# Kernel optimization log

Hardware: AMD Instinct MI355X
Metric: run time of the kernel (lower is better)

The kernel has to match this reference:

```python
import jax, jax.numpy as jnp
import numpy as np

D_MODEL = 512
N_HEADS = 8
HEAD_DIM = D_MODEL // N_HEADS
KV_RANK = 128
B, T = 8, 4096


def _rope(x):
    # x: (B, H, T, D); non-interleaved half rotation as in the source
    d = x.shape[-1]
    half = d // 2
    freq = 1.0 / (10000.0 ** (jnp.arange(half, dtype=jnp.float32) / half))
    t = jnp.arange(x.shape[2], dtype=jnp.float32)
    freqs = jnp.einsum('i,j->ij', t, freq)          # (T, half)
    cos_f = jnp.cos(freqs)[None, None, :, :]
    sin_f = jnp.sin(freqs)[None, None, :, :]
    x1, x2 = jnp.split(x, 2, axis=-1)
    return jnp.concatenate([x1 * cos_f - x2 * sin_f, x1 * sin_f + x2 * cos_f], axis=-1)


def setup_inputs() -> dict:
    key = jax.random.key(0)
    ks = jax.random.split(key, 9)
    s = lambda fan_in: 1.0 / np.sqrt(fan_in)
    return {
        'x':  jax.random.normal(ks[0], (B, T, D_MODEL), dtype=jnp.float32),
        'Wq': jax.random.normal(ks[1], (D_MODEL, D_MODEL), dtype=jnp.float32) * s(D_MODEL),
        'bq': jnp.zeros((D_MODEL,), dtype=jnp.float32),
        'Wd': jax.random.normal(ks[2], (D_MODEL, KV_RANK), dtype=jnp.float32) * s(D_MODEL),
        'bd': jnp.zeros((KV_RANK,), dtype=jnp.float32),
        'Wu': jax.random.normal(ks[3], (KV_RANK, D_MODEL * 2), dtype=jnp.float32) * s(KV_RANK),
        'bu': jnp.zeros((D_MODEL * 2,), dtype=jnp.float32),
        'Wo': jax.random.normal(ks[4], (D_MODEL, D_MODEL), dtype=jnp.float32) * s(D_MODEL),
        'bo': jnp.zeros((D_MODEL,), dtype=jnp.float32),
    }


def reference(x, Wq, bq, Wd, bd, Wu, bu, Wo, bo):
    b, t, _ = x.shape
    q = (x @ Wq + bq).reshape(b, t, N_HEADS, HEAD_DIM).transpose(0, 2, 1, 3)   # (B,H,T,D)
    kv = ((x @ Wd + bd) @ Wu + bu).reshape(b, t, N_HEADS, 2 * HEAD_DIM)
    k, v = jnp.split(kv, 2, axis=-1)
    k = k.transpose(0, 2, 1, 3)                                                # (B,H,T,D)
    v = v.transpose(0, 2, 1, 3)
    q = jax.nn.elu(_rope(q)) + 1.0
    k = jax.nn.elu(_rope(k)) + 1.0
    context = jnp.einsum('bhtd,bhte->bhde', k, v)      # (B,H,D,D)
    out = jnp.einsum('bhtd,bhde->bhte', q, context)    # (B,H,T,D)
    k_sum = k.sum(axis=2)                              # (B,H,D)
    z = 1.0 / (jnp.einsum('bhtd,bhd->bht', q, k_sum) + 1e-6)
    out = out * z[..., None]
    out = out.transpose(0, 2, 1, 3).reshape(b, t, D_MODEL)
    return out @ Wo + bo
```

## Files before the change

### kernel.cpp

```cpp
#include <hip/hip_runtime.h>
#include <math.h>

#define T_SEQ 4096
#define BATCH 8
#define DM    512
#define NH    8
#define HD    64
#define RANK  128
#define NCHUNK 8
#define MTOT  (BATCH * T_SEQ)
#define BK 64

typedef unsigned int u32;
typedef unsigned short u16;
using bf16x8  = __attribute__((ext_vector_type(8))) __bf16;
using floatx4 = __attribute__((ext_vector_type(4))) float;

__device__ __forceinline__ u16 f2bf(float f) {
  u32 u = __float_as_uint(f);
  u32 r = (u + 0x7FFFu + ((u >> 16) & 1u)) >> 16;
  return (u16)r;
}
__device__ __forceinline__ void hilo(float f, u16& h, u16& l) {
  h = f2bf(f);
  float hf = __uint_as_float(((u32)h) << 16);
  l = f2bf(f - hf);
}
__device__ __forceinline__ float elu1(float x) {
  return (x > 0.f) ? x + 1.f : expf(x);
}
__device__ __forceinline__ void async16(void* lds, const void* g) {
  __builtin_amdgcn_global_load_lds(
      (const __attribute__((address_space(1))) u32*)g,
      (__attribute__((address_space(3))) u32*)lds, 16, 0, 0);
}
__device__ __forceinline__ bf16x8 fragld(const u16* base, int row, int kk, int quad) {
  int ch = (kk * 4 + quad) ^ (row & 7);
  return *(const bf16x8*)((const char*)base + row * 128 + ch * 16);
}
__device__ __forceinline__ bf16x8 fragldA(const u16* base, int row, int gc) {
  int ch = gc ^ (row & 7);
  return *(const bf16x8*)((const char*)base + row * 256 + ch * 16);
}

__global__ void cs_kernel(float2* __restrict__ cs) {
  int i = blockIdx.x * 256 + threadIdx.x;
  if (i >= T_SEQ * 32) return;
  int t = i >> 5, d = i & 31;
  double freq = pow(10000.0, -(double)d / 32.0);
  double a = (double)t * freq;
  cs[i] = make_float2((float)cos(a), (float)sin(a));
}

__global__ __launch_bounds__(256) void pack_bf16(const float* __restrict__ x,
                                                 u16* __restrict__ y) {
  int i = blockIdx.x * 256 + threadIdx.x;
  const float4 v = ((const float4*)x)[i];
  ushort4 o;
  o.x = f2bf(v.x); o.y = f2bf(v.y); o.z = f2bf(v.z); o.w = f2bf(v.w);
  ((ushort4*)y)[i] = o;
}

__global__ __launch_bounds__(256) void transpose_cast(const float* __restrict__ W,
                                                      u16* __restrict__ WT,
                                                      int K, int N) {
  __shared__ float t[32][33];
  int kb = blockIdx.x * 32, nb = blockIdx.y * 32;
  int tx = threadIdx.x & 31, tg = threadIdx.x >> 5;
#pragma unroll
  for (int i = 0; i < 4; i++)
    t[tg * 4 + i][tx] = W[(size_t)(kb + tg * 4 + i) * N + nb + tx];
  __syncthreads();
#pragma unroll
  for (int i = 0; i < 4; i++)
    WT[(size_t)(nb + tg * 4 + i) * K + kb + tx] = f2bf(t[tx][tg * 4 + i]);
}

__global__ __launch_bounds__(256) void transpose_cast_hilo(
    const float* __restrict__ W, u16* __restrict__ WTh, u16* __restrict__ WTl,
    int K, int N) {
  __shared__ float t[32][33];
  int kb = blockIdx.x * 32, nb = blockIdx.y * 32;
  int tx = threadIdx.x & 31, tg = threadIdx.x >> 5;
#pragma unroll
  for (int i = 0; i < 4; i++)
    t[tg * 4 + i][tx] = W[(size_t)(kb + tg * 4 + i) * N + nb + tx];
  __syncthreads();
#pragma unroll
  for (int i = 0; i < 4; i++) {
    u16 h, l;
    hilo(t[tx][tg * 4 + i], h, l);
    WTh[(size_t)(nb + tg * 4 + i) * K + kb + tx] = h;
    WTl[(size_t)(nb + tg * 4 + i) * K + kb + tx] = l;
  }
}

template <bool BF16OUT>
__global__ __launch_bounds__(256) void gemm_bf16_bt(
    const u16* __restrict__ A, const u16* __restrict__ BT,
    const float* __restrict__ bias, void* __restrict__ Cv,
    int M, int N, int K) {
  __shared__ u16 As[128 * BK];
  __shared__ u16 Bs[128 * BK];
  const int tid = threadIdx.x;
  const int lane = tid & 63, w = tid >> 6;
  const int m0 = blockIdx.y * 128, n0 = blockIdx.x * 128;
  const int wm = (w & 1) * 64, wn = (w >> 1) * 64;
  const int srow = lane >> 3, schunk = lane & 7;
  const int lane15 = lane & 15, quad = lane >> 4;
  floatx4 acc[4][4] = {};
  for (int kt = 0; kt < K; kt += BK) {
    __syncthreads();
#pragma unroll
    for (int i = 0; i < 4; i++) {
      int R = (w * 4 + i) * 8 + srow;
      int cg = schunk ^ (R & 7);
      async16((char*)As + (w * 4 + i) * 1024,
              (const char*)A + ((size_t)(m0 + R) * K + kt) * 2 + cg * 16);
      async16((char*)Bs + (w * 4 + i) * 1024,
              (const char*)BT + ((size_t)(n0 + R) * K + kt) * 2 + cg * 16);
    }
    __syncthreads();
#pragma unroll
    for (int kk = 0; kk < 2; kk++) {
      bf16x8 af[4], bfr[4];
#pragma unroll
      for (int mi = 0; mi < 4; mi++) af[mi] = fragld(As, wm + mi * 16 + lane15, kk, quad);
#pragma unroll
      for (int ni = 0; ni < 4; ni++) bfr[ni] = fragld(Bs, wn + ni * 16 + lane15, kk, quad);
#pragma unroll
      for (int mi = 0; mi < 4; mi++)
#pragma unroll
        for (int ni = 0; ni < 4; ni++)
          acc[mi][ni] = __builtin_amdgcn_mfma_f32_16x16x32_bf16(
              af[mi], bfr[ni], acc[mi][ni], 0, 0, 0);
    }
  }
#pragma unroll
  for (int mi = 0; mi < 4; mi++) {
    int row = m0 + wm + mi * 16 + (quad << 2);
#pragma unroll
    for (int ni = 0; ni < 4; ni++) {
      int col = n0 + wn + ni * 16 + lane15;
      float bb = bias[col];
#pragma unroll
      for (int r = 0; r < 4; r++) {
        float v = acc[mi][ni][r] + bb;
        if (BF16OUT) ((u16*)Cv)[(size_t)(row + r) * N + col] = f2bf(v);
        else         ((float*)Cv)[(size_t)(row + r) * N + col] = v;
      }
    }
  }
}

__global__ __launch_bounds__(256) void gemm_wd_hilo(
    const u16* __restrict__ A, const u16* __restrict__ BT,
    const float* __restrict__ bias, u16* __restrict__ Ch, u16* __restrict__ Cl,
    int M, int N, int K) {
  __shared__ u16 As[128 * BK];
  __shared__ u16 Bs[128 * BK];
  const int tid = threadIdx.x;
  const int lane = tid & 63, w = tid >> 6;
  const int m0 = blockIdx.y * 128, n0 = blockIdx.x * 128;
  const int wm = (w & 1) * 64, wn = (w >> 1) * 64;
  const int srow = lane >> 3, schunk = lane & 7;
  const int lane15 = lane & 15, quad = lane >> 4;
  floatx4 acc[4][4] = {};
  for (int kt = 0; kt < K; kt += BK) {
    __syncthreads();
#pragma unroll
    for (int i = 0; i < 4; i++) {
      int R = (w * 4 + i) * 8 + srow;
      int cg = schunk ^ (R & 7);
      async16((char*)As + (w * 4 + i) * 1024,
              (const char*)A + ((size_t)(m0 + R) * K + kt) * 2 + cg * 16);
      async16((char*)Bs + (w * 4 + i) * 1024,
              (const char*)BT + ((size_t)(n0 + R) * K + kt) * 2 + cg * 16);
    }
    __syncthreads();
#pragma unroll
    for (int kk = 0; kk < 2; kk++) {
      bf16x8 af[4], bfr[4];
#pragma unroll
      for (int mi = 0; mi < 4; mi++) af[mi] = fragld(As, wm + mi * 16 + lane15, kk, quad);
#pragma unroll
      for (int ni = 0; ni < 4; ni++) bfr[ni] = fragld(Bs, wn + ni * 16 + lane15, kk, quad);
#pragma unroll
      for (int mi = 0; mi < 4; mi++)
#pragma unroll
        for (int ni = 0; ni < 4; ni++)
          acc[mi][ni] = __builtin_amdgcn_mfma_f32_16x16x32_bf16(
              af[mi], bfr[ni], acc[mi][ni], 0, 0, 0);
    }
  }
#pragma unroll
  for (int mi = 0; mi < 4; mi++) {
    int row = m0 + wm + mi * 16 + (quad << 2);
#pragma unroll
    for (int ni = 0; ni < 4; ni++) {
      int col = n0 + wn + ni * 16 + lane15;
      float bb = bias[col];
#pragma unroll
      for (int r = 0; r < 4; r++) {
        float v = acc[mi][ni][r] + bb;
        u16 hh, ll;
        hilo(v, hh, ll);
        size_t idx = (size_t)(row + r) * N + col;
        Ch[idx] = hh;
        Cl[idx] = ll;
      }
    }
  }
}

__global__ __launch_bounds__(256, 2) void ctx_fused(
    const u16* __restrict__ Chi, const u16* __restrict__ Clo,
    const u16* __restrict__ Wuh, const u16* __restrict__ Wul,
    const float* __restrict__ bu, const float2* __restrict__ cs,
    float* __restrict__ ctxp, float* __restrict__ ksump) {
  __shared__ __align__(16) u16 Ah_[64 * 128];
  __shared__ __align__(16) u16 Al_[64 * 128];
  __shared__ __align__(16) u16 Kh_[64 * 64], Kl_[64 * 64];
  __shared__ __align__(16) u16 Vh_[64 * 64], Vl_[64 * 64];
  __shared__ float bus[128];
  __shared__ float ksl[256];
  const int tid = threadIdx.x;
  const int lane = tid & 63, w = tid >> 6;
  const int lane15 = lane & 15, quad = lane >> 4;
  const int chunk = blockIdx.x, bh = blockIdx.y;
  const int b = bh >> 3, h = bh & 7;
  if (tid < 128) bus[tid] = bu[h * RANK + tid];

  bf16x8 wuh[2][2][2], wul[2][2][2];
  {
    const int cb = (w >> 1) * 4 + (w & 1);
#pragma unroll
    for (int rp = 0; rp < 2; rp++)
#pragma unroll
      for (int kk = 0; kk < 2; kk++)
#pragma unroll
        for (int ct = 0; ct < 2; ct++) {
          size_t off = (size_t)(h * 128 + (cb + ct * 2) * 16 + lane15) * RANK
                       + rp * 64 + kk * 32 + quad * 8;
          wuh[rp][kk][ct] = *(const bf16x8*)(Wuh + off);
          wul[rp][kk][ct] = *(const bf16x8*)(Wul + off);
        }
  }

  const int t00 = chunk * 512;
  auto stageA = [&](int t0) {
#pragma unroll
    for (int i = 0; i < 4; i++) {
      int R = i * 16 + w * 4 + (lane >> 4);
      int cg = (lane & 15) ^ (R & 7);
      size_t aoff = ((size_t)(b * T_SEQ + t0 + R) * RANK + cg * 8) * 2;
      async16((char*)Ah_ + (i * 16 + w * 4) * 256, (const char*)Chi + aoff);
      async16((char*)Al_ + (i * 16 + w * 4) * 256, (const char*)Clo + aoff);
    }
  };

  floatx4 acc2[4] = {};
  float ks0 = 0.f, ks1 = 0.f;
  stageA(t00);
  for (int tile = 0; tile < 8; tile++) {
    const int t0 = t00 + tile * 64;
    __syncthreads();
    floatx4 acc[4][2] = {};
#pragma unroll
    for (int rp = 0; rp < 2; rp++)
#pragma unroll
      for (int kk = 0; kk < 2; kk++) {
        const int gc = rp * 8 + kk * 4 + quad;
        bf16x8 ah[4], al[4];
#pragma unroll
        for (int tt = 0; tt < 4; tt++) {
          ah[tt] = fragldA(Ah_, tt * 16 + lane15, gc);
          al[tt] = fragldA(Al_, tt * 16 + lane15, gc);
        }
#pragma unroll
        for (int tt = 0; tt < 4; tt++)
#pragma unroll
          for (int ct = 0; ct < 2; ct++) {
            acc[tt][ct] = __builtin_amdgcn_mfma_f32_16x16x32_bf16(
                ah[tt], wuh[rp][kk][ct], acc[tt][ct], 0, 0, 0);
            acc[tt][ct] = __builtin_amdgcn_mfma_f32_16x16x32_bf16(
                ah[tt], wul[rp][kk][ct], acc[tt][ct], 0, 0, 0);
            acc[tt][ct] = __builtin_amdgcn_mfma_f32_16x16x32_bf16(
                al[tt], wuh[rp][kk][ct], acc[tt][ct], 0, 0, 0);
            acc[tt][ct] = __builtin_amdgcn_mfma_f32_16x16x32_bf16(
                al[tt], wul[rp][kk][ct], acc[tt][ct], 0, 0, 0);
          }
      }
    __syncthreads();
    if (tile < 7) stageA(t0 + 64);
    if (w < 2) {
      const int d = w * 16 + lane15;
      const float b1 = bus[d], b2 = bus[d + 32];
#pragma unroll
      for (int tt = 0; tt < 4; tt++) {
        const int tg = t0 + tt * 16 + (quad << 2);
        ushort4 khl, kll, khh, klh;
        float s0 = 0.f, s1 = 0.f;
#pragma unroll
        for (int r = 0; r < 4; r++) {
          float2 sc = cs[(size_t)(tg + r) * 32 + d];
          float x1 = acc[tt][0][r] + b1;
          float x2 = acc[tt][1][r] + b2;
          float k1 = elu1(x1 * sc.x - x2 * sc.y);
          float k2 = elu1(x1 * sc.y + x2 * sc.x);
          s0 += k1; s1 += k2;
          u16 hh, ll;
          hilo(k1, hh, ll); ((u16*)&khl)[r] = hh; ((u16*)&kll)[r] = ll;
          hilo(k2, hh, ll); ((u16*)&khh)[r] = hh; ((u16*)&klh)[r] = ll;
        }
        ks0 += s0; ks1 += s1;
        const int chq = tt * 2 + (quad >> 1);
        const int off = d * 128 + (((chq ^ (d & 7)) << 4) | ((quad & 1) << 3));
        *(ushort4*)((char*)Kh_ + off)            = khl;
        *(ushort4*)((char*)Kl_ + off)            = kll;
        *(ushort4*)((char*)Kh_ + off + 32 * 128) = khh;
        *(ushort4*)((char*)Kl_ + off + 32 * 128) = klh;
      }
    } else {
      const int e = (w - 2) * 16 + lane15;
#pragma unroll
      for (int ct = 0; ct < 2; ct++) {
        const float be = bus[64 + e + ct * 32];
#pragma unroll
        for (int tt = 0; tt < 4; tt++) {
          ushort4 vh4, vl4;
#pragma unroll
          for (int r = 0; r < 4; r++) {
            u16 hh, ll;
            hilo(acc[tt][ct][r] + be, hh, ll);
            ((u16*)&vh4)[r] = hh; ((u16*)&vl4)[r] = ll;
          }
          const int chq = tt * 2 + (quad >> 1);
          const int off = (e + ct * 32) * 128 +
                          (((chq ^ (e & 7)) << 4) | ((quad & 1) << 3));
          *(ushort4*)((char*)Vh_ + off) = vh4;
          *(ushort4*)((char*)Vl_ + off) = vl4;
        }
      }
    }
    __syncthreads();
#pragma unroll
    for (int kk = 0; kk < 2; kk++) {
      bf16x8 kh8 = fragld(Kh_, w * 16 + lane15, kk, quad);
      bf16x8 kl8 = fragld(Kl_, w * 16 + lane15, kk, quad);
#pragma unroll
      for (int ni = 0; ni < 4; ni++) {
        bf16x8 vh8 = fragld(Vh_, ni * 16 + lane15, kk, quad);
        bf16x8 vl8 = fragld(Vl_, ni * 16 + lane15, kk, quad);
        acc2[ni] = __builtin_amdgcn_mfma_f32_16x16x32_bf16(kh8, vh8, acc2[ni], 0, 0, 0);
        acc2[ni] = __builtin_amdgcn_mfma_f32_16x16x32_bf16(kh8, vl8, acc2[ni], 0, 0, 0);
        acc2[ni] = __builtin_amdgcn_mfma_f32_16x16x32_bf16(kl8, vh8, acc2[ni], 0, 0, 0);
        acc2[ni] = __builtin_amdgcn_mfma_f32_16x16x32_bf16(kl8, vl8, acc2[ni], 0, 0, 0);
      }
    }
  }
  const size_t obase = ((size_t)bh * NCHUNK + chunk) * 4096;
#pragma unroll
  for (int ni = 0; ni < 4; ni++)
#pragma unroll
    for (int r = 0; r < 4; r++)
      ctxp[obase + (size_t)(w * 16 + (quad << 2) + r) * 64 + ni * 16 + lane15] = acc2[ni][r];
  if (w < 2) {
    ksl[w * 128 + lane]      = ks0;
    ksl[w * 128 + 64 + lane] = ks1;
  }
  __syncthreads();
  if (tid < 64) {
    const int d = tid;
    const int wk = (d >> 4) & 1, hi = d >> 5, l15 = d & 15;
    float s = 0.f;
#pragma unroll
    for (int q = 0; q < 4; q++) s += ksl[wk * 128 + hi * 64 + q * 16 + l15];
    ksump[(bh * NCHUNK + chunk) * 64 + d] = s;
  }
}

__global__ __launch_bounds__(256) void reduce_kernel(
    const float* __restrict__ ctxp, const float* __restrict__ ksump,
    float* __restrict__ ctx, float* __restrict__ ksum) {
  int bh = blockIdx.x, tid = threadIdx.x;
  for (int i = tid; i < 4096; i += 256) {
    float s = 0.f;
    for (int c = 0; c < NCHUNK; c++) s += ctxp[(size_t)(bh * NCHUNK + c) * 4096 + i];
    ctx[(size_t)bh * 4096 + i] = s;
  }
  if (tid < 64) {
    float s = 0.f;
    for (int c = 0; c < NCHUNK; c++) s += ksump[(bh * NCHUNK + c) * 64 + tid];
    ksum[bh * 64 + tid] = s;
  }
}

__global__ __launch_bounds__(256) void out_kernel(
    const float* __restrict__ Q, const float* __restrict__ ctx,
    const float* __restrict__ ksum, const float2* __restrict__ cs,
    u16* __restrict__ attn) {
  __shared__ __align__(16) float Qs[128 * 68];
  __shared__ __align__(16) float Cts[64 * 68];
  __shared__ float ks[64];
  __shared__ float zs[128];
  const int tid = threadIdx.x;
  const int tt0 = blockIdx.x * 128;
  const int bh = blockIdx.y;
  const int b = bh >> 3, h = bh & 7;
  for (int i = tid; i < 4096; i += 256)
    Cts[(i >> 6) * 68 + (i & 63)] = ctx[(size_t)bh * 4096 + i];
  if (tid < 64) ks[tid] = ksum[bh * 64 + tid];
  for (int i = tid; i < 8192; i += 256) {
    int t = i >> 6, d = i & 63;
    Qs[t * 68 + d] = Q[(size_t)(b * T_SEQ + tt0 + t) * DM + h * HD + d];
  }
  __syncthreads();
  for (int i = tid; i < 128 * 32; i += 256) {
    int t = i >> 5, d = i & 31;
    float x1 = Qs[t * 68 + d], x2 = Qs[t * 68 + d + 32];
    float2 sc = cs[(size_t)(tt0 + t) * 32 + d];
    float r1 = x1 * sc.x - x2 * sc.y;
    float r2 = x1 * sc.y + x2 * sc.x;
    Qs[t * 68 + d]      = (r1 > 0.f) ? r1 + 1.f : expf(r1);
    Qs[t * 68 + d + 32] = (r2 > 0.f) ? r2 + 1.f : expf(r2);
  }
  __syncthreads();
  if (tid < 128) {
    float z = 0.f;
#pragma unroll 8
    for (int d = 0; d < 64; d++) z += Qs[tid * 68 + d] * ks[d];
    zs[tid] = 1.f / (z + 1e-6f);
  }
  __syncthreads();
  const int tx = tid & 15, ty = tid >> 4;
  float acc[8][4] = {};
  for (int d = 0; d < 64; d++) {
    const float4 c4 = *(const float4*)&Cts[d * 68 + tx * 4];
#pragma unroll
    for (int i = 0; i < 8; i++) {
      float q = Qs[(ty * 8 + i) * 68 + d];
      acc[i][0] += q * c4.x; acc[i][1] += q * c4.y;
      acc[i][2] += q * c4.z; acc[i][3] += q * c4.w;
    }
  }
#pragma unroll
  for (int i = 0; i < 8; i++) {
    int t = ty * 8 + i;
    float zz = zs[t];
    ushort4 o;
    o.x = f2bf(acc[i][0] * zz); o.y = f2bf(acc[i][1] * zz);
    o.z = f2bf(acc[i][2] * zz); o.w = f2bf(acc[i][3] * zz);
    *(ushort4*)&attn[(size_t)(b * T_SEQ + tt0 + t) * DM + h * HD + tx * 4] = o;
  }
}

extern "C" void kernel_launch(void* const* d_in, const int* in_sizes, int n_in,
                              void* d_out, int out_size, void* d_ws, size_t ws_size,
                              hipStream_t stream) {
  const float* x  = (const float*)d_in[0];
  const float* Wq = (const float*)d_in[1];
  const float* bq = (const float*)d_in[2];
  const float* Wd = (const float*)d_in[3];
  const float* bd = (const float*)d_in[4];
  const float* Wu = (const float*)d_in[5];
  const float* bu = (const float*)d_in[6];
  const float* Wo = (const float*)d_in[7];
  const float* bo = (const float*)d_in[8];
  float* out = (float*)d_out;

  float* ws = (float*)d_ws;
  size_t o_cs   = 0;
  size_t o_Q    = o_cs + (size_t)T_SEQ * 32 * 2;
  size_t o_Chi  = o_Q + (size_t)MTOT * DM;
  size_t o_Clo  = o_Chi + (size_t)MTOT * RANK / 2;
  size_t o_ctxp = o_Clo + (size_t)MTOT * RANK / 2;
  size_t o_ksp  = o_ctxp + (size_t)64 * NCHUNK * 4096;
  size_t o_ctx  = o_ksp + (size_t)64 * NCHUNK * 64;
  size_t o_ks   = o_ctx + (size_t)64 * 4096;
  size_t o_xbf  = o_ks + 64 * 64;
  size_t o_wqT  = o_xbf + (size_t)MTOT * DM / 2;
  size_t o_wdT  = o_wqT + (size_t)DM * DM / 2;
  size_t o_woT  = o_wdT + (size_t)DM * RANK / 2;
  size_t o_wuTh = o_woT + (size_t)DM * DM / 2;
  size_t o_wuTl = o_wuTh + (size_t)(2 * DM) * RANK / 2;
  size_t total  = o_wuTl + (size_t)(2 * DM) * RANK / 2;
  if (ws_size < total * sizeof(float)) return;

  float2* cs  = (float2*)(ws + o_cs);
  float* Qb   = ws + o_Q;
  u16* Chi    = (u16*)(ws + o_Chi);
  u16* Clo    = (u16*)(ws + o_Clo);
  float* ctxp = ws + o_ctxp;
  float* ksp  = ws + o_ksp;
  float* ctxf = ws + o_ctx;
  float* ksf  = ws + o_ks;
  u16* x_bf   = (u16*)(ws + o_xbf);
  u16* attn_bf= x_bf;
  u16* WqT    = (u16*)(ws + o_wqT);
  u16* WdT    = (u16*)(ws + o_wdT);
  u16* WoT    = (u16*)(ws + o_woT);
  u16* WuTh   = (u16*)(ws + o_wuTh);
  u16* WuTl   = (u16*)(ws + o_wuTl);

  cs_kernel<<<(T_SEQ * 32 + 255) / 256, 256, 0, stream>>>(cs);
  pack_bf16<<<(MTOT * DM / 4) / 256, 256, 0, stream>>>(x, x_bf);
  transpose_cast<<<dim3(DM / 32, DM / 32), 256, 0, stream>>>(Wq, WqT, DM, DM);
  transpose_cast<<<dim3(DM / 32, RANK / 32), 256, 0, stream>>>(Wd, WdT, DM, RANK);
  transpose_cast<<<dim3(DM / 32, DM / 32), 256, 0, stream>>>(Wo, WoT, DM, DM);
  transpose_cast_hilo<<<dim3(RANK / 32, (2 * DM) / 32), 256, 0, stream>>>(
      Wu, WuTh, WuTl, RANK, 2 * DM);

  gemm_bf16_bt<false><<<dim3(DM / 128, MTOT / 128), 256, 0, stream>>>(
      x_bf, WqT, bq, Qb, MTOT, DM, DM);
  gemm_wd_hilo<<<dim3(RANK / 128, MTOT / 128), 256, 0, stream>>>(
      x_bf, WdT, bd, Chi, Clo, MTOT, RANK, DM);
  ctx_fused<<<dim3(NCHUNK, BATCH * NH), 256, 0, stream>>>(
      Chi, Clo, WuTh, WuTl, bu, cs, ctxp, ksp);
  reduce_kernel<<<BATCH * NH, 256, 0, stream>>>(ctxp, ksp, ctxf, ksf);
  out_kernel<<<dim3(T_SEQ / 128, BATCH * NH), 256, 0, stream>>>(Qb, ctxf, ksf, cs, attn_bf);
  gemm_bf16_bt<false><<<dim3(DM / 128, MTOT / 128), 256, 0, stream>>>(
      attn_bf, WoT, bo, out, MTOT, DM, DM);
}
```

Measured before the change: 332.8 us.

## Split context kernel into more chunks, halve A staging, drop lo*lo MFMAs

Doubles the number of sequence chunks in the fused context kernel and processes each 64-row tile as two 32-row halves with a smaller shared A buffer, raising the occupancy hint from two to three blocks per CU. It also drops the low-by-low product terms from both the Wu projection and the K^T V accumulation, cutting MFMA work by a quarter. The partial-context buffer now aliases the x_bf16 workspace. This trades a small loss in split-precision accuracy, extra barriers and a larger reduction for more parallelism and less matrix work; the aliasing assumes x_bf is dead by the time ctx_fused runs.

```diff
diff --git a/kernel.cpp b/kernel.cpp
--- a/kernel.cpp
+++ b/kernel.cpp
@@ -7,7 +7,7 @@
 #define NH    8
 #define HD    64
 #define RANK  128
-#define NCHUNK 8
+#define NCHUNK 16
 #define MTOT  (BATCH * T_SEQ)
 #define BK 64
 
@@ -213,13 +213,13 @@
   }
 }
 
-__global__ __launch_bounds__(256, 2) void ctx_fused(
+__global__ __launch_bounds__(256, 3) void ctx_fused(
     const u16* __restrict__ Chi, const u16* __restrict__ Clo,
     const u16* __restrict__ Wuh, const u16* __restrict__ Wul,
     const float* __restrict__ bu, const float2* __restrict__ cs,
     float* __restrict__ ctxp, float* __restrict__ ksump) {
-  __shared__ __align__(16) u16 Ah_[64 * 128];
-  __shared__ __align__(16) u16 Al_[64 * 128];
+  __shared__ __align__(16) u16 Ah_[32 * 128];
+  __shared__ __align__(16) u16 Al_[32 * 128];
   __shared__ __align__(16) u16 Kh_[64 * 64], Kl_[64 * 64];
   __shared__ __align__(16) u16 Vh_[64 * 64], Vl_[64 * 64];
   __shared__ float bus[128];
@@ -247,13 +247,13 @@
         }
   }
 
-  const int t00 = chunk * 512;
-  auto stageA = [&](int t0) {
-#pragma unroll
-    for (int i = 0; i < 4; i++) {
+  const int t00 = chunk * (T_SEQ / NCHUNK);
+  auto stageA = [&](int tg0) {
+#pragma unroll
+    for (int i = 0; i < 2; i++) {
       int R = i * 16 + w * 4 + (lane >> 4);
       int cg = (lane & 15) ^ (R & 7);
-      size_t aoff = ((size_t)(b * T_SEQ + t0 + R) * RANK + cg * 8) * 2;
+      size_t aoff = ((size_t)(b * T_SEQ + tg0 + R) * RANK + cg * 8) * 2;
       async16((char*)Ah_ + (i * 16 + w * 4) * 256, (const char*)Chi + aoff);
       async16((char*)Al_ + (i * 16 + w * 4) * 256, (const char*)Clo + aoff);
     }
@@ -262,84 +262,87 @@
   floatx4 acc2[4] = {};
   float ks0 = 0.f, ks1 = 0.f;
   stageA(t00);
-  for (int tile = 0; tile < 8; tile++) {
+  for (int tile = 0; tile < T_SEQ / NCHUNK / 64; tile++) {
     const int t0 = t00 + tile * 64;
-    __syncthreads();
-    floatx4 acc[4][2] = {};
-#pragma unroll
-    for (int rp = 0; rp < 2; rp++)
-#pragma unroll
-      for (int kk = 0; kk < 2; kk++) {
-        const int gc = rp * 8 + kk * 4 + quad;
-        bf16x8 ah[4], al[4];
-#pragma unroll
-        for (int tt = 0; tt < 4; tt++) {
-          ah[tt] = fragldA(Ah_, tt * 16 + lane15, gc);
-          al[tt] = fragldA(Al_, tt * 16 + lane15, gc);
+#pragma unroll
+    for (int hh = 0; hh < 2; hh++) {
+      __syncthreads();
+      floatx4 acc[2][2] = {};
+#pragma unroll
+      for (int rp = 0; rp < 2; rp++)
+#pragma unroll
+        for (int kk = 0; kk < 2; kk++) {
+          const int gc = rp * 8 + kk * 4 + quad;
+          bf16x8 ah[2], al[2];
+#pragma unroll
+          for (int tt = 0; tt < 2; tt++) {
+            ah[tt] = fragldA(Ah_, tt * 16 + lane15, gc);
+            al[tt] = fragldA(Al_, tt * 16 + lane15, gc);
+          }
+#pragma unroll
+          for (int tt = 0; tt < 2; tt++)
+#pragma unroll
+            for (int ct = 0; ct < 2; ct++) {
+              acc[tt][ct] = __builtin_amdgcn_mfma_f32_16x16x32_bf16(
+                  ah[tt], wuh[rp][kk][ct], acc[tt][ct], 0, 0, 0);
+              acc[tt][ct] = __builtin_amdgcn_mfma_f32_16x16x32_bf16(
+                  ah[tt], wul[rp][kk][ct], acc[tt][ct], 0, 0, 0);
+              acc[tt][ct] = __builtin_amdgcn_mfma_f32_16x16x32_bf16(
+                  al[tt], wuh[rp][kk][ct], acc[tt][ct], 0, 0, 0);
+            }
         }
-#pragma unroll
-        for (int tt = 0; tt < 4; tt++)
-#pragma unroll
-          for (int ct = 0; ct < 2; ct++) {
-            acc[tt][ct] = __builtin_amdgcn_mfma_f32_16x16x32_bf16(
-                ah[tt], wuh[rp][kk][ct], acc[tt][ct], 0, 0, 0);
-            acc[tt][ct] = __builtin_amdgcn_mfma_f32_16x16x32_bf16(
-                ah[tt], wul[rp][kk][ct], acc[tt][ct], 0, 0, 0);
-            acc[tt][ct] = __builtin_amdgcn_mfma_f32_16x16x32_bf16(
-                al[tt], wuh[rp][kk][ct], acc[tt][ct], 0, 0, 0);
-            acc[tt][ct] = __builtin_amdgcn_mfma_f32_16x16x32_bf16(
-                al[tt], wul[rp][kk][ct], acc[tt][ct], 0, 0, 0);
+      __syncthreads();
+      if (hh == 0) stageA(t0 + 32);
+      else if (tile < T_SEQ / NCHUNK / 64 - 1) stageA(t0 + 64);
+      const int tbase = t0 + hh * 32;
+      if (w < 2) {
+        const int d = w * 16 + lane15;
+        const float b1 = bus[d], b2 = bus[d + 32];
+#pragma unroll
+        for (int tt = 0; tt < 2; tt++) {
+          const int tg = tbase + tt * 16 + (quad << 2);
+          ushort4 khl, kll, khh, klh;
+          float s0 = 0.f, s1 = 0.f;
+#pragma unroll
+          for (int r = 0; r < 4; r++) {
+            float2 sc = cs[(size_t)(tg + r) * 32 + d];
+            float x1 = acc[tt][0][r] + b1;
+            float x2 = acc[tt][1][r] + b2;
+            float k1 = elu1(x1 * sc.x - x2 * sc.y);
+            float k2 = elu1(x1 * sc.y + x2 * sc.x);
+            s0 += k1; s1 += k2;
+            u16 hh_, ll_;
+            hilo(k1, hh_, ll_); ((u16*)&khl)[r] = hh_; ((u16*)&kll)[r] = ll_;
+            hilo(k2, hh_, ll_); ((u16*)&khh)[r] = hh_; ((u16*)&klh)[r] = ll_;
           }
-      }
-    __syncthreads();
-    if (tile < 7) stageA(t0 + 64);
-    if (w < 2) {
-      const int d = w * 16 + lane15;
-      const float b1 = bus[d], b2 = bus[d + 32];
-#pragma unroll
-      for (int tt = 0; tt < 4; tt++) {
-        const int tg = t0 + tt * 16 + (quad << 2);
-        ushort4 khl, kll, khh, klh;
-        float s0 = 0.f, s1 = 0.f;
-#pragma unroll
-        for (int r = 0; r < 4; r++) {
-          float2 sc = cs[(size_t)(tg + r) * 32 + d];
-          float x1 = acc[tt][0][r] + b1;
-          float x2 = acc[tt][1][r] + b2;
-          float k1 = elu1(x1 * sc.x - x2 * sc.y);
-          float k2 = elu1(x1 * sc.y + x2 * sc.x);
-          s0 += k1; s1 += k2;
-          u16 hh, ll;
-          hilo(k1, hh, ll); ((u16*)&khl)[r] = hh; ((u16*)&kll)[r] = ll;
-          hilo(k2, hh, ll); ((u16*)&khh)[r] = hh; ((u16*)&klh)[r] = ll;
+          ks0 += s0; ks1 += s1;
+          const int chq = hh * 4 + tt * 2 + (quad >> 1);
+          const int off = d * 128 + (((chq ^ (d & 7)) << 4) | ((quad & 1) << 3));
+          *(ushort4*)((char*)Kh_ + off)            = khl;
+          *(ushort4*)((char*)Kl_ + off)            = kll;
+          *(ushort4*)((char*)Kh_ + off + 32 * 128) = khh;
+          *(ushort4*)((char*)Kl_ + off + 32 * 128) = klh;
         }
-        ks0 += s0; ks1 += s1;
-        const int chq = tt * 2 + (quad >> 1);
-        const int off = d * 128 + (((chq ^ (d & 7)) << 4) | ((quad & 1) << 3));
-        *(ushort4*)((char*)Kh_ + off)            = khl;
-        *(ushort4*)((char*)Kl_ + off)            = kll;
-        *(ushort4*)((char*)Kh_ + off + 32 * 128) = khh;
-        *(ushort4*)((char*)Kl_ + off + 32 * 128) = klh;
-      }
-    } else {
-      const int e = (w - 2) * 16 + lane15;
-#pragma unroll
-      for (int ct = 0; ct < 2; ct++) {
-        const float be = bus[64 + e + ct * 32];
-#pragma unroll
-        for (int tt = 0; tt < 4; tt++) {
-          ushort4 vh4, vl4;
-#pragma unroll
-          for (int r = 0; r < 4; r++) {
-            u16 hh, ll;
-            hilo(acc[tt][ct][r] + be, hh, ll);
-            ((u16*)&vh4)[r] = hh; ((u16*)&vl4)[r] = ll;
+      } else {
+        const int e = (w - 2) * 16 + lane15;
+#pragma unroll
+        for (int ct = 0; ct < 2; ct++) {
+          const float be = bus[64 + e + ct * 32];
+#pragma unroll
+          for (int tt = 0; tt < 2; tt++) {
+            ushort4 vh4, vl4;
+#pragma unroll
+            for (int r = 0; r < 4; r++) {
+              u16 hh_, ll_;
+              hilo(acc[tt][ct][r] + be, hh_, ll_);
+              ((u16*)&vh4)[r] = hh_; ((u16*)&vl4)[r] = ll_;
+            }
+            const int chq = hh * 4 + tt * 2 + (quad >> 1);
+            const int off = (e + ct * 32) * 128 +
+                            (((chq ^ (e & 7)) << 4) | ((quad & 1) << 3));
+            *(ushort4*)((char*)Vh_ + off) = vh4;
+            *(ushort4*)((char*)Vl_ + off) = vl4;
           }
-          const int chq = tt * 2 + (quad >> 1);
-          const int off = (e + ct * 32) * 128 +
-                          (((chq ^ (e & 7)) << 4) | ((quad & 1) << 3));
-          *(ushort4*)((char*)Vh_ + off) = vh4;
-          *(ushort4*)((char*)Vl_ + off) = vl4;
         }
       }
     }
@@ -355,7 +358,6 @@
         acc2[ni] = __builtin_amdgcn_mfma_f32_16x16x32_bf16(kh8, vh8, acc2[ni], 0, 0, 0);
         acc2[ni] = __builtin_amdgcn_mfma_f32_16x16x32_bf16(kh8, vl8, acc2[ni], 0, 0, 0);
         acc2[ni] = __builtin_amdgcn_mfma_f32_16x16x32_bf16(kl8, vh8, acc2[ni], 0, 0, 0);
-        acc2[ni] = __builtin_amdgcn_mfma_f32_16x16x32_bf16(kl8, vl8, acc2[ni], 0, 0, 0);
       }
     }
   }
@@ -474,8 +476,7 @@
   size_t o_Q    = o_cs + (size_t)T_SEQ * 32 * 2;
   size_t o_Chi  = o_Q + (size_t)MTOT * DM;
   size_t o_Clo  = o_Chi + (size_t)MTOT * RANK / 2;
-  size_t o_ctxp = o_Clo + (size_t)MTOT * RANK / 2;
-  size_t o_ksp  = o_ctxp + (size_t)64 * NCHUNK * 4096;
+  size_t o_ksp  = o_Clo + (size_t)MTOT * RANK / 2;
   size_t o_ctx  = o_ksp + (size_t)64 * NCHUNK * 64;
   size_t o_ks   = o_ctx + (size_t)64 * 4096;
   size_t o_xbf  = o_ks + 64 * 64;
@@ -491,12 +492,12 @@
   float* Qb   = ws + o_Q;
   u16* Chi    = (u16*)(ws + o_Chi);
   u16* Clo    = (u16*)(ws + o_Clo);
-  float* ctxp = ws + o_ctxp;
   float* ksp  = ws + o_ksp;
   float* ctxf = ws + o_ctx;
   float* ksf  = ws + o_ks;
   u16* x_bf   = (u16*)(ws + o_xbf);
   u16* attn_bf= x_bf;
+  float* ctxp = ws + o_xbf;
   u16* WqT    = (u16*)(ws + o_wqT);
   u16* WdT    = (u16*)(ws + o_wdT);
   u16* WoT    = (u16*)(ws + o_woT);
```

After: 324.7 us. 2.4% less time.
